# Performance work log

Hardware: AMD Instinct MI355X
Metric: run time of the kernel (lower is better)

## Reference

```python
import jax, jax.numpy as jnp
import numpy as np

N, DIN, DOUT = 8192, 128, 128
NEG = -9.0e15  # the module's -9000000000000000.0 mask value
ALPHA = 0.2    # LeakyReLU negative slope


def setup_inputs() -> dict:
    key = jax.random.key(0)
    kx, ka, kw, ks, kr = jax.random.split(key, 5)
    X = jax.random.normal(kx, (N, DIN), dtype=jnp.float32)
    A = (jax.random.uniform(ka, (N, N)) < 0.01).astype(jnp.float32)
    A = A.at[jnp.arange(N), jnp.arange(N)].set(1.0)
    # Linear weight (Kaiming-uniform-ish range is irrelevant to math; use Xavier)
    lim_w = float(np.sqrt(6.0 / (DIN + DOUT)))
    W = jax.random.uniform(kw, (DOUT, DIN), jnp.float32, -lim_w, lim_w)
    b = jnp.zeros((DOUT,), jnp.float32)
    lim_a = float(np.sqrt(6.0 / (DOUT + 1)))
    a_s = jax.random.uniform(ks, (DOUT, 1), jnp.float32, -lim_a, lim_a)
    a_r = jax.random.uniform(kr, (DOUT, 1), jnp.float32, -lim_a, lim_a)
    return {"X": X, "A": A, "W": W, "b": b, "a_s": a_s, "a_r": a_r}


def reference(X, A, W, b, a_s, a_r):
    # H_in = Linear(X)
    H = X @ W.T + b                         # [N, DOUT]
    s = H @ a_s                             # [N, 1] source scores
    r = H @ a_r                             # [N, 1] receiver scores
    # M_s = A * s (broadcast over cols), M_r = A * r^T (broadcast over rows)
    e = jax.nn.leaky_relu(A * s + A * r.T, negative_slope=ALPHA)  # [N, N]
    masked = jnp.where(A > 0, e, NEG)
    att = jax.nn.softmax(masked, axis=1)    # row-stochastic attention
    H_out = att @ H                         # [N, DOUT]  (act = Identity, dropout = eval)
    # NOTE: the torch module applies LayerNorm into a local var but returns
    # the pre-norm H_out, so LayerNorm is dead code. A and [] passthroughs omitted.
    return H_out
```

## Files before the change

kernel.cpp:

```cpp
#include <hip/hip_runtime.h>

#define N 8192
#define D 128
#define ALPHA 0.2f
#define RCAP 256

__global__ __launch_bounds__(256) void linear_kernel(
    const float* __restrict__ X, const float* __restrict__ W,
    const float* __restrict__ b, const float* __restrict__ a_s,
    const float* __restrict__ a_r,
    float* __restrict__ H, float* __restrict__ sv, float* __restrict__ rv)
{
    __shared__ float Xs[128 * 36];
    __shared__ float Ws[64 * 132];

    const int tid = threadIdx.x;
    const int i0  = blockIdx.x * 32;

    for (int idx = tid; idx < 32 * 128; idx += 256) {
        const int row = idx >> 7, k = idx & 127;
        Xs[k * 36 + row] = X[(i0 + row) * D + k];
    }

    float acc[4][4] = {};
    const int ty = tid >> 5, tx = tid & 31;
    const int rbase = ty * 4, cbase = tx * 4;

    for (int kb = 0; kb < 2; ++kb) {
        __syncthreads();
        for (int idx = tid; idx < 64 * 128; idx += 256) {
            const int o = idx >> 6, kk = idx & 63;
            Ws[kk * 132 + o] = W[o * D + kb * 64 + kk];
        }
        __syncthreads();
        #pragma unroll
        for (int kk = 0; kk < 64; ++kk) {
            const float4 xv = *(const float4*)&Xs[(kb * 64 + kk) * 36 + rbase];
            const float4 wv = *(const float4*)&Ws[kk * 132 + cbase];
            const float xr[4] = {xv.x, xv.y, xv.z, xv.w};
            const float wc[4] = {wv.x, wv.y, wv.z, wv.w};
            #pragma unroll
            for (int r = 0; r < 4; ++r)
                #pragma unroll
                for (int c = 0; c < 4; ++c)
                    acc[r][c] += xr[r] * wc[c];
        }
    }

    const float4 bv  = *(const float4*)&b[cbase];
    const float4 asv = *(const float4*)&a_s[cbase];
    const float4 arv = *(const float4*)&a_r[cbase];
    #pragma unroll
    for (int r = 0; r < 4; ++r) {
        float4 h;
        h.x = acc[r][0] + bv.x;
        h.y = acc[r][1] + bv.y;
        h.z = acc[r][2] + bv.z;
        h.w = acc[r][3] + bv.w;
        *(float4*)&H[(size_t)(i0 + rbase + r) * D + cbase] = h;
        float ps = h.x * asv.x + h.y * asv.y + h.z * asv.z + h.w * asv.w;
        float pr = h.x * arv.x + h.y * arv.y + h.z * arv.z + h.w * arv.w;
        #pragma unroll
        for (int off = 16; off > 0; off >>= 1) {
            ps += __shfl_xor(ps, off);
            pr += __shfl_xor(pr, off);
        }
        if (tx == 0) {
            sv[i0 + rbase + r] = ps;
            rv[i0 + rbase + r] = pr;
        }
    }
}

__global__ __launch_bounds__(256, 8) void attn_fused(
    const float* __restrict__ A, const float* __restrict__ H,
    const float* __restrict__ sv, const float* __restrict__ rv,
    float* __restrict__ out)
{
    __shared__ float2 s_l[4][RCAP];

    const int wave = threadIdx.x >> 6;
    const int lane = threadIdx.x & 63;
    const int i    = blockIdx.x * 4 + wave;
    const unsigned long long lt = (1ull << lane) - 1ull;

    const float4* __restrict__ Arow = (const float4*)(A + (size_t)i * N);

    int cnt = 0;
    float4 cur = Arow[lane];
    #pragma unroll 1
    for (int it = 0; it < 32; ++it) {
        float4 nxt = make_float4(0.f, 0.f, 0.f, 0.f);
        if (it < 31) nxt = Arow[(it + 1) * 64 + lane];
        const int col0 = it * 256 + lane * 4;
        const float av[4] = {cur.x, cur.y, cur.z, cur.w};
        #pragma unroll
        for (int e = 0; e < 4; ++e) {
            const bool nz = (av[e] != 0.0f);
            const unsigned long long m = __ballot(nz);
            if (nz) {
                const int pos = cnt + __popcll(m & lt);
                if (pos < RCAP) s_l[wave][pos].y = __int_as_float(col0 + e);
            }
            cnt += __popcll(m);
        }
        cur = nxt;
    }
    cnt = (cnt < RCAP) ? cnt : RCAP;

    const float si = sv[i];
    float zv[4];
    #pragma unroll
    for (int k = 0; k < 4; ++k) {
        const int p = lane + 64 * k;
        const bool act = (p < cnt);
        const int j = act ? __float_as_int(s_l[wave][p].y) : 0;
        float z = si + rv[j];
        z = (z > 0.0f) ? z : ALPHA * z;
        zv[k] = act ? z : -3.0e38f;
    }
    float lm = fmaxf(fmaxf(zv[0], zv[1]), fmaxf(zv[2], zv[3]));
    #pragma unroll
    for (int off = 32; off > 0; off >>= 1) lm = fmaxf(lm, __shfl_xor(lm, off));

    float sl = 0.0f;
    float wv4[4];
    #pragma unroll
    for (int k = 0; k < 4; ++k) {
        const int p = lane + 64 * k;
        const float w = (p < cnt) ? __expf(zv[k] - lm) : 0.0f;
        wv4[k] = w;
        sl += w;
    }
    #pragma unroll
    for (int off = 32; off > 0; off >>= 1) sl += __shfl_xor(sl, off);
    const float inv = 1.0f / sl;

    #pragma unroll
    for (int k = 0; k < 4; ++k) {
        const int p = lane + 64 * k;
        if (p < cnt) s_l[wave][p].x = wv4[k] * inv;
    }

    float2 acc = make_float2(0.0f, 0.0f);
    const float* __restrict__ Hl = H + 2 * lane;
    #pragma unroll 4
    for (int p = 0; p < cnt; ++p) {
        const float2 wj = s_l[wave][p];
        const int   j  = __float_as_int(wj.y);
        const float2 h = *(const float2*)&Hl[(size_t)j * D];
        acc.x += wj.x * h.x;
        acc.y += wj.x * h.y;
    }
    *(float2*)&out[(size_t)i * D + 2 * lane] = acc;
}

extern "C" void kernel_launch(void* const* d_in, const int* in_sizes, int n_in,
                              void* d_out, int out_size, void* d_ws, size_t ws_size,
                              hipStream_t stream) {
    const float* X   = (const float*)d_in[0];
    const float* A   = (const float*)d_in[1];
    const float* W   = (const float*)d_in[2];
    const float* b   = (const float*)d_in[3];
    const float* a_s = (const float*)d_in[4];
    const float* a_r = (const float*)d_in[5];
    float* out = (float*)d_out;

    float* H  = (float*)d_ws;
    float* sv = H + (size_t)N * D;
    float* rv = sv + N;

    linear_kernel<<<256, 256, 0, stream>>>(X, W, b, a_s, a_r, H, sv, rv);
    attn_fused<<<N / 4, 256, 0, stream>>>(A, H, sv, rv, out);
}
```

Baseline: 402.4 us.

## Deepen A-row prefetch and compact nonzeros via per-lane bitmask scan

The attention kernel now loads four float4s of the adjacency row per lane per iteration with double buffering, so 4 KB per wave is in flight instead of one float4. Each lane builds a 16-bit nonzero mask and the wave runs an inclusive shuffle-up prefix sum to find output slots, replacing per-element ballots. The aim is more memory-level parallelism on the 256 MB A stream and fewer cross-lane ops. In exchange it uses more registers, so the occupancy hint is lowered from 8 to 6, and adds a per-lane serial loop over set bits.

Result: slower. 446.7 us (+11.0%).

```diff
diff --git a/kernel.cpp b/kernel.cpp
--- a/kernel.cpp
+++ b/kernel.cpp
@@ -72,7 +72,7 @@
     }
 }
 
-__global__ __launch_bounds__(256, 8) void attn_fused(
+__global__ __launch_bounds__(256, 6) void attn_fused(
     const float* __restrict__ A, const float* __restrict__ H,
     const float* __restrict__ sv, const float* __restrict__ rv,
     float* __restrict__ out)
@@ -82,29 +82,48 @@
     const int wave = threadIdx.x >> 6;
     const int lane = threadIdx.x & 63;
     const int i    = blockIdx.x * 4 + wave;
-    const unsigned long long lt = (1ull << lane) - 1ull;
 
     const float4* __restrict__ Arow = (const float4*)(A + (size_t)i * N);
 
+    float4 buf[2][4];
+    #pragma unroll
+    for (int q = 0; q < 4; ++q) buf[0][q] = Arow[q * 64 + lane];
+
     int cnt = 0;
-    float4 cur = Arow[lane];
     #pragma unroll 1
-    for (int it = 0; it < 32; ++it) {
-        float4 nxt = make_float4(0.f, 0.f, 0.f, 0.f);
-        if (it < 31) nxt = Arow[(it + 1) * 64 + lane];
-        const int col0 = it * 256 + lane * 4;
-        const float av[4] = {cur.x, cur.y, cur.z, cur.w};
+    for (int it = 0; it < 8; ++it) {
+        const int cb = it & 1;
+        if (it < 7) {
+            #pragma unroll
+            for (int q = 0; q < 4; ++q)
+                buf[cb ^ 1][q] = Arow[(it + 1) * 256 + q * 64 + lane];
+        }
+        unsigned m = 0;
         #pragma unroll
-        for (int e = 0; e < 4; ++e) {
-            const bool nz = (av[e] != 0.0f);
-            const unsigned long long m = __ballot(nz);
-            if (nz) {
-                const int pos = cnt + __popcll(m & lt);
-                if (pos < RCAP) s_l[wave][pos].y = __int_as_float(col0 + e);
-            }
-            cnt += __popcll(m);
+        for (int q = 0; q < 4; ++q) {
+            const float4 a = buf[cb][q];
+            m |= (a.x != 0.0f ? 1u : 0u) << (q * 4 + 0);
+            m |= (a.y != 0.0f ? 1u : 0u) << (q * 4 + 1);
+            m |= (a.z != 0.0f ? 1u : 0u) << (q * 4 + 2);
+            m |= (a.w != 0.0f ? 1u : 0u) << (q * 4 + 3);
         }
-        cur = nxt;
+        const int c = __popc(m);
+        int scan = c;
+        #pragma unroll
+        for (int off = 1; off < 64; off <<= 1) {
+            const int t = __shfl_up(scan, off);
+            if (lane >= off) scan += t;
+        }
+        int base = cnt + scan - c;
+        cnt += __shfl(scan, 63);
+        while (m) {
+            const int k = __ffs(m) - 1;
+            m &= m - 1;
+            const int q = k >> 2, e = k & 3;
+            if (base < RCAP)
+                s_l[wave][base].y = __int_as_float(it * 1024 + q * 256 + lane * 4 + e);
+            ++base;
+        }
     }
     cnt = (cnt < RCAP) ? cnt : RCAP;
 
```
